# Optimization experiments

Hardware: AMD Instinct MI355X
Metric: run time of the kernel (lower is better)

Reference implementation:

```python
import jax, jax.numpy as jnp
import numpy as np

B, C, H, W = 1, 512, 64, 64
HEADS, DIM_HEAD = 8, 64
GROUPS = 32
EPS = 1e-5
SCALE = DIM_HEAD ** -0.5


def setup_inputs() -> dict:
    key = jax.random.key(0)
    ks = jax.random.split(key, 8)
    inner = HEADS * DIM_HEAD  # 512
    s = 0.02
    return {
        "hidden_states": jax.random.normal(ks[0], (B, C, H, W), jnp.float32),
        "gn_gamma": jnp.ones((C,), jnp.float32),
        "gn_beta": jnp.zeros((C,), jnp.float32),
        "wq": jax.random.normal(ks[1], (inner, C), jnp.float32) * s,
        "wk": jax.random.normal(ks[2], (inner, C), jnp.float32) * s,
        "wv": jax.random.normal(ks[3], (inner, C), jnp.float32) * s,
        "wo": jax.random.normal(ks[4], (C, inner), jnp.float32) * s,
        "bo": jnp.zeros((C,), jnp.float32),
    }


def _group_norm(x, gamma, beta):
    # x: [B, C, H, W]; normalize within channel groups over (C//G, H, W)
    b, c, h, w = x.shape
    xg = x.reshape(b, GROUPS, c // GROUPS, h, w)
    mean = xg.mean(axis=(2, 3, 4), keepdims=True)
    var = xg.var(axis=(2, 3, 4), keepdims=True)
    xg = (xg - mean) * jax.lax.rsqrt(var + EPS)
    x = xg.reshape(b, c, h, w)
    return x * gamma[None, :, None, None] + beta[None, :, None, None]


def reference(hidden_states, gn_gamma, gn_beta, wq, wk, wv, wo, bo):
    residual = hidden_states
    x = _group_norm(hidden_states, gn_gamma, gn_beta)
    b, c, h, w = x.shape
    n = h * w
    x = x.reshape(b, c, n).transpose(0, 2, 1)  # [B, N, C]

    # torch Linear: y = x @ W^T (bias=False for q/k/v)
    q = (x @ wq.T).reshape(b, n, HEADS, DIM_HEAD).transpose(0, 2, 1, 3)  # [B,H,N,D]
    k = (x @ wk.T).reshape(b, n, HEADS, DIM_HEAD).transpose(0, 2, 1, 3)
    v = (x @ wv.T).reshape(b, n, HEADS, DIM_HEAD).transpose(0, 2, 1, 3)

    scores = jnp.einsum("bhqd,bhkd->bhqk", q, k) * SCALE  # [B,H,N,N]
    probs = jax.nn.softmax(scores, axis=-1)
    out = jnp.einsum("bhqk,bhkd->bhqd", probs, v)  # [B,H,N,D]

    out = out.transpose(0, 2, 1, 3).reshape(b, n, HEADS * DIM_HEAD)  # [B,N,inner]
    out = out @ wo.T + bo  # [B,N,C]
    out = out.transpose(0, 2, 1).reshape(b, c, h, w)
    return out + residual
```

## Files before the change

kernel.cpp:

```cpp
#include <hip/hip_runtime.h>

#define N_TOK 4096
#define C_DIM 512
#define NH    8
#define EPS   1e-5f
#define NSPLIT 4
#define THR   11.0f

typedef __attribute__((ext_vector_type(8))) __bf16 bf16x8;
typedef __attribute__((ext_vector_type(4))) float  f32x4;
using u16 = unsigned short;
using u32 = unsigned int;

#define MFMA16 __builtin_amdgcn_mfma_f32_16x16x32_bf16

__device__ __forceinline__ u16 f2bf(float f){
  u32 x = __builtin_bit_cast(u32, f);
  x += 0x7fffu + ((x>>16)&1u);
  return (u16)(x>>16);
}
__device__ __forceinline__ float bf2f(u16 v){
  return __builtin_bit_cast(float, (u32)v<<16);
}
__device__ __forceinline__ float exp2a(float x){
  float r; asm("v_exp_f32 %0, %1" : "=v"(r) : "v"(x)); return r;
}
__device__ __forceinline__ u32 cvtpk(float lo, float hi){
  u32 r; asm("v_cvt_pk_bf16_f32 %0, %1, %2" : "=v"(r) : "v"(lo), "v"(hi)); return r;
}
__device__ __forceinline__ float max3a(float a, float b, float c){
  float r; asm("v_max3_f32 %0, %1, %2, %3" : "=v"(r) : "v"(a), "v"(b), "v"(c)); return r;
}
__device__ __forceinline__ void dma16(const void* src, void* lds){
  __builtin_amdgcn_global_load_lds(
      (const __attribute__((address_space(1))) u32*)src,
      (__attribute__((address_space(3))) u32*)lds, 16, 0, 0);
}

__global__ __launch_bounds__(256) void k_pre(const float* __restrict__ s0,
      const float* __restrict__ s1, const float* __restrict__ s2,
      const float* __restrict__ s3, u16* __restrict__ d0, u16* __restrict__ d1,
      u16* __restrict__ d2, u16* __restrict__ d3,
      const float* __restrict__ x, float* __restrict__ pstat,
      u16* __restrict__ xbf){
  __shared__ float rs[4], rss[4];
  int b = blockIdx.x;
  if (b < 1024){
    int m = b >> 8;
    int i = (b & 255)*256 + threadIdx.x;
    const float* s = m==0?s0 : m==1?s1 : m==2?s2 : s3;
    u16*         d = m==0?d0 : m==1?d1 : m==2?d2 : d3;
    float4 v = ((const float4*)s)[i];
    ushort4 o; o.x=f2bf(v.x); o.y=f2bf(v.y); o.z=f2bf(v.z); o.w=f2bf(v.w);
    ((ushort4*)d)[i] = o;
    return;
  }
  int gb = b - 1024;
  int g = gb>>3, p = gb&7, t = threadIdx.x;
  const float4* gx4 = (const float4*)(x + (size_t)g*16*N_TOK) + (size_t)p*2048;
  ushort4* xb4 = (ushort4*)xbf + (size_t)g*16384 + (size_t)p*2048;
  float s=0.f, ss=0.f;
  #pragma unroll
  for (int k=0;k<8;k++){
    float4 v = gx4[t + k*256];
    s  += v.x+v.y+v.z+v.w;
    ss += v.x*v.x+v.y*v.y+v.z*v.z+v.w*v.w;
    ushort4 o; o.x=f2bf(v.x); o.y=f2bf(v.y); o.z=f2bf(v.z); o.w=f2bf(v.w);
    xb4[t + k*256] = o;
  }
  for (int m=1;m<64;m<<=1){ s += __shfl_xor(s,m); ss += __shfl_xor(ss,m); }
  int w=t>>6, lane=t&63;
  if (lane==0){ rs[w]=s; rss[w]=ss; }
  __syncthreads();
  if (t==0){
    pstat[(g*8+p)*2  ] = rs[0]+rs[1]+rs[2]+rs[3];
    pstat[(g*8+p)*2+1] = rss[0]+rss[1]+rss[2]+rss[3];
  }
}

__global__ __launch_bounds__(256) void k_gn_apply(const u16* __restrict__ xbf,
      const float* __restrict__ pstat, const float* __restrict__ gamma,
      const float* __restrict__ beta, u16* __restrict__ X){
  int g = blockIdx.x, c0 = g*16;
  int n = blockIdx.y*256 + threadIdx.x;
  float S=0.f, SS=0.f;
  #pragma unroll
  for (int p=0;p<8;p++){ S += pstat[(g*8+p)*2]; SS += pstat[(g*8+p)*2+1]; }
  float mean = S*(1.f/65536.f);
  float rstd = rsqrtf(SS*(1.f/65536.f) - mean*mean + EPS);
  u16 ov[16];
  #pragma unroll
  for (int c=0;c<16;c++){
    float gm = gamma[c0+c]*rstd;
    float be = beta[c0+c] - mean*gm;
    float v  = bf2f(xbf[(size_t)(c0+c)*N_TOK + n])*gm + be;
    ov[c] = f2bf(v);
  }
  uint4* dst = (uint4*)&X[(size_t)n*C_DIM + c0];
  dst[0] = *(uint4*)&ov[0];
  dst[1] = *(uint4*)&ov[8];
}

__device__ __forceinline__ void gemm_core64(const u16* A, const u16* B,
      int m0, int n0, char* LDS, f32x4 (&acc)[4][2]){
  int t = threadIdx.x, w = t>>6, l = t&63, lr = l&15, li = l>>4;
  int wr = w>>1, wc = w&1;
  char* As = LDS;
  char* Bs = LDS + 32768;
  const char* Ac = (const char*)A + (size_t)m0*1024;
  const char* Bc = (const char*)B + (size_t)n0*1024;
  int rswz = (lr&7)<<4;

  int rowA[4], segA[4], rowB[2], segB[2];
  #pragma unroll
  for (int k=0;k<4;k++){ int s=t+k*256; rowA[k]=s>>3; segA[k]=s&7; }
  #pragma unroll
  for (int k=0;k<2;k++){ int s=t+k*256; rowB[k]=s>>3; segB[k]=s&7; }

  #define STAGE(it, bb) { int koff=(it)*128;                                   \
    _Pragma("unroll")                                                          \
    for (int k=0;k<4;k++){                                                     \
      int ys = (segA[k]*16) ^ ((rowA[k]&7)<<4);                                \
      dma16(Ac + (size_t)rowA[k]*1024 + koff + ys,                             \
            As + (bb)*16384 + w*1024 + k*4096);                                \
    }                                                                          \
    _Pragma("unroll")                                                          \
    for (int k=0;k<2;k++){                                                     \
      int ys = (segB[k]*16) ^ ((rowB[k]&7)<<4);                                \
      dma16(Bc + (size_t)rowB[k]*1024 + koff + ys,                             \
            Bs + (bb)*8192 + w*1024 + k*4096);                                 \
    } }

  STAGE(0, 0);
  __syncthreads();

  int buf = 0;
  for (int it=0; it<8; it++){
    if (it < 7){ STAGE(it+1, buf^1); }
    char* Ab = As + buf*16384;
    char* Bb = Bs + buf*8192;
    #pragma unroll
    for (int ks=0; ks<2; ks++){
      bf16x8 af[4], bfr[2];
      #pragma unroll
      for (int i=0;i<4;i++){
        int ra = wr*64 + i*16 + lr;
        af[i]  = *(const bf16x8*)(Ab + ra*128 + ((li*16 + ks*64) ^ rswz));
      }
      #pragma unroll
      for (int j=0;j<2;j++){
        int rb = wc*32 + j*16 + lr;
        bfr[j] = *(const bf16x8*)(Bb + rb*128 + ((li*16 + ks*64) ^ rswz));
      }
      __builtin_amdgcn_s_setprio(1);
      #pragma unroll
      for (int i=0;i<4;i++){
        #pragma unroll
        for (int j=0;j<2;j++){
          acc[i][j] = MFMA16(af[i], bfr[j], acc[i][j], 0,0,0);
        }
      }
      __builtin_amdgcn_s_setprio(0);
    }
    __syncthreads();
    buf ^= 1;
  }
  #undef STAGE
}

__global__ __launch_bounds__(256,3) void k_qkv2(const u16* __restrict__ X,
      const u16* __restrict__ wq, const u16* __restrict__ wk,
      const u16* __restrict__ wv, u16* __restrict__ Qo, u16* __restrict__ Ko,
      u16* __restrict__ Vto){
  __shared__ char LDS[49152];
  int b = blockIdx.x;
  const u16 *A, *B; u16* Cp; int ldc, m0, n0; float sc = 1.f; bool vperm = false;
  if (b < 256){        A=X;  B=wq; Cp=Qo;  ldc=512;  m0=(b>>3)*128; n0=(b&7)*64;
                       sc = 0.125f*1.44269504f; }
  else if (b < 512){ int r=b-256; A=X;  B=wk; Cp=Ko;  ldc=512;  m0=(r>>3)*128; n0=(r&7)*64; }
  else             { int r=b-512; A=wv; B=X;  Cp=Vto; ldc=4096; m0=(r>>6)*128; n0=(r&63)*64;
                     vperm = true; }

  f32x4 acc[4][2] = {};
  gemm_core64(A, B, m0, n0, LDS, acc);

  int t = threadIdx.x, w = t>>6, l = t&63, lr = l&15, li = l>>4;
  int wr = w>>1, wc = w&1;
  #pragma unroll
  for (int i=0;i<4;i++){
    #pragma unroll
    for (int rr=0;rr<4;rr++){
      int mm = m0 + wr*64 + i*16 + li*4 + rr;
      #pragma unroll
      for (int j=0;j<2;j++){
        int nn = n0 + wc*32 + j*16 + lr;
        if (vperm){
          int tl = nn & 63;
          int pos = (tl & 35) | ((tl & 12) << 1) | ((tl & 16) >> 2);
          nn = (nn & ~63) | pos;
        }
        Cp[(size_t)mm*ldc + nn] = f2bf(acc[i][j][rr]*sc);
      }
    }
  }
}

__global__ __launch_bounds__(256,3) void k_oproj2(const u16* __restrict__ Wo,
      const u16* __restrict__ Ob, const float* __restrict__ bo,
      const float* __restrict__ res, float* __restrict__ out){
  __shared__ char LDS[49152];
  int b = blockIdx.x;
  int m0 = (b>>6)*128, n0 = (b&63)*64;

  f32x4 acc[4][2] = {};
  gemm_core64(Wo, Ob, m0, n0, LDS, acc);

  int t = threadIdx.x, w = t>>6, l = t&63, lr = l&15, li = l>>4;
  int wr = w>>1, wc = w&1;
  #pragma unroll
  for (int i=0;i<4;i++){
    #pragma unroll
    for (int rr=0;rr<4;rr++){
      int cc = m0 + wr*64 + i*16 + li*4 + rr;
      float bias = bo[cc];
      #pragma unroll
      for (int j=0;j<2;j++){
        int nn = n0 + wc*32 + j*16 + lr;
        size_t off = (size_t)cc*4096 + nn;
        out[off] = acc[i][j][rr] + bias + res[off];
      }
    }
  }
}

__global__ __launch_bounds__(256,4) void k_attn6(const u16* __restrict__ Q,
      const u16* __restrict__ K, const u16* __restrict__ Vt,
      u16* __restrict__ Opart, float* __restrict__ ml){
  __shared__ char KV[2][16384];
  int b = blockIdx.x;
  int xcd  = b & 7;
  int slot = b >> 3;
  int pair = xcd*4 + (slot >> 5);
  int h  = pair & 7;
  int sp = pair >> 3;
  int q0 = (slot & 31) * 128;
  int t = threadIdx.x, w = t>>6, l = t&63, lr = l&15, li = l>>4;
  char* KVb = (char*)KV;
  int qbase = q0 + w*32;

  const u16* Qp = Q + (size_t)(qbase + lr)*512 + h*64 + li*8;
  bf16x8 qa00 = *(const bf16x8*)(Qp);
  bf16x8 qa01 = *(const bf16x8*)(Qp + 32);
  bf16x8 qa10 = *(const bf16x8*)(Qp + 16*512);
  bf16x8 qa11 = *(const bf16x8*)(Qp + 16*512 + 32);

  int srow = l>>3, y0 = (l&7)*16;
  const char* Kc = (const char*)K;
  const char* Vc = (const char*)Vt;
  const char* ksrc[2]; const char* vsrc[2]; int ldso[2];
  #pragma unroll
  for (int j=0;j<2;j++){
    int row = w*16 + j*8 + srow;
    int ys  = y0 ^ ((row&7)<<4);
    ksrc[j] = Kc + (size_t)(sp*1024 + row)*1024 + h*128 + ys;
    vsrc[j] = Vc + (size_t)(h*64 + row)*8192 + sp*2048 + ys;
    ldso[j] = w*2048 + j*1024;
  }

  #pragma unroll
  for (int j=0;j<2;j++){
    dma16(ksrc[j], KVb + ldso[j]);
    dma16(vsrc[j], KVb + 8192 + ldso[j]);
  }
  __syncthreads();

  f32x4 acc0[4] = {}; f32x4 acc1[4] = {};
  float m0=-1e30f, m1=-1e30f, l0=0.f, l1=0.f;
  int buf = 0;

  for (int it=0; it<16; it++){
    if (it < 15){
      int nb = buf^1;
      #pragma unroll
      for (int j=0;j<2;j++){
        dma16(ksrc[j] + (size_t)(it+1)*65536, KVb + nb*16384 + ldso[j]);
        dma16(vsrc[j] + (it+1)*128,           KVb + nb*16384 + 8192 + ldso[j]);
      }
    }
    char* Klb = KVb + buf*16384;
    char* Vlb = Klb + 8192;

    f32x4 st0[4] = {}; f32x4 st1[4] = {};
    __builtin_amdgcn_s_setprio(1);
    #pragma unroll
    for (int T=0;T<4;T++){
      int row = T*16 + lr, swz = (row&7)<<4;
      const char* rb = Klb + row*128;
      bf16x8 k0 = *(const bf16x8*)(rb + ((li*16     ) ^ swz));
      bf16x8 k1 = *(const bf16x8*)(rb + ((li*16 + 64) ^ swz));
      st0[T] = MFMA16(k0, qa00, st0[T], 0,0,0);
      st0[T] = MFMA16(k1, qa01, st0[T], 0,0,0);
      st1[T] = MFMA16(k0, qa10, st1[T], 0,0,0);
      st1[T] = MFMA16(k1, qa11, st1[T], 0,0,0);
    }
    __builtin_amdgcn_s_setprio(0);

    u32 pk0[8], pk1[8];
    {
      float a0 = max3a(st0[0][0],st0[0][1],st0[0][2]);
      float a1 = max3a(st0[1][0],st0[1][1],st0[1][2]);
      float a2 = max3a(st0[2][0],st0[2][1],st0[2][2]);
      float a3 = max3a(st0[3][0],st0[3][1],st0[3][2]);
      float b0 = max3a(st0[0][3],st0[1][3],st0[2][3]);
      float pmax = fmaxf(max3a(a0,a1,a2), max3a(a3,b0,st0[3][3]));
      pmax = fmaxf(pmax, __shfl_xor(pmax,16));
      pmax = fmaxf(pmax, __shfl_xor(pmax,32));
      if (!__all(pmax <= m0 + THR)){
        float mnew = fmaxf(m0, pmax);
        float fac = exp2a(m0 - mnew);
        m0 = mnew; l0 *= fac;
        float f0=__shfl(fac, li*20+0), f1=__shfl(fac, li*20+1);
        float f2=__shfl(fac, li*20+2), f3=__shfl(fac, li*20+3);
        #pragma unroll
        for (int T=0;T<4;T++){
          acc0[T][0]*=f0; acc0[T][1]*=f1; acc0[T][2]*=f2; acc0[T][3]*=f3;
        }
      }
      float lad = 0.f;
      #pragma unroll
      for (int T=0;T<4;T++){
        float p0=exp2a(st0[T][0]-m0), p1=exp2a(st0[T][1]-m0);
        float p2=exp2a(st0[T][2]-m0), p3=exp2a(st0[T][3]-m0);
        lad += (p0+p1)+(p2+p3);
        pk0[T*2]   = cvtpk(p0,p1);
        pk0[T*2+1] = cvtpk(p2,p3);
      }
      l0 += lad;
    }
    {
      float a0 = max3a(st1[0][0],st1[0][1],st1[0][2]);
      float a1 = max3a(st1[1][0],st1[1][1],st1[1][2]);
      float a2 = max3a(st1[2][0],st1[2][1],st1[2][2]);
      float a3 = max3a(st1[3][0],st1[3][1],st1[3][2]);
      float b0 = max3a(st1[0][3],st1[1][3],st1[2][3]);
      float pmax = fmaxf(max3a(a0,a1,a2), max3a(a3,b0,st1[3][3]));
      pmax = fmaxf(pmax, __shfl_xor(pmax,16));
      pmax = fmaxf(pmax, __shfl_xor(pmax,32));
      if (!__all(pmax <= m1 + THR)){
        float mnew = fmaxf(m1, pmax);
        float fac = exp2a(m1 - mnew);
        m1 = mnew; l1 *= fac;
        float f0=__shfl(fac, li*20+0), f1=__shfl(fac, li*20+1);
        float f2=__shfl(fac, li*20+2), f3=__shfl(fac, li*20+3);
        #pragma unroll
        for (int T=0;T<4;T++){
          acc1[T][0]*=f0; acc1[T][1]*=f1; acc1[T][2]*=f2; acc1[T][3]*=f3;
        }
      }
      float lad = 0.f;
      #pragma unroll
      for (int T=0;T<4;T++){
        float p0=exp2a(st1[T][0]-m1), p1=exp2a(st1[T][1]-m1);
        float p2=exp2a(st1[T][2]-m1), p3=exp2a(st1[T][3]-m1);
        lad += (p0+p1)+(p2+p3);
        pk1[T*2]   = cvtpk(p0,p1);
        pk1[T*2+1] = cvtpk(p2,p3);
      }
      l1 += lad;
    }

    __builtin_amdgcn_s_setprio(1);
    #pragma unroll
    for (int c=0;c<2;c++){
      union { bf16x8 v; u32 u[4]; } A0, A1;
      #pragma unroll
      for (int k=0;k<4;k++){ A0.u[k]=pk0[c*4+k]; A1.u[k]=pk1[c*4+k]; }
      #pragma unroll
      for (int T=0;T<4;T++){
        int vrow = T*16 + lr, vswz = (vrow&7)<<4;
        bf16x8 vb = *(const bf16x8*)(Vlb + vrow*128 + ((c*64 + li*16) ^ vswz));
        acc0[T] = MFMA16(A0.v, vb, acc0[T], 0,0,0);
        acc1[T] = MFMA16(A1.v, vb, acc1[T], 0,0,0);
      }
    }
    __builtin_amdgcn_s_setprio(0);

    __syncthreads();
    buf ^= 1;
  }

  l0 += __shfl_xor(l0,16); l0 += __shfl_xor(l0,32);
  l1 += __shfl_xor(l1,16); l1 += __shfl_xor(l1,32);
  u16* Op = Opart + (size_t)sp*N_TOK*C_DIM;
  #pragma unroll
  for (int T=0;T<4;T++){
    #pragma unroll
    for (int r=0;r<4;r++){
      Op[(size_t)(qbase      + li*4 + r)*512 + h*64 + T*16 + lr] = f2bf(acc0[T][r]);
      Op[(size_t)(qbase + 16 + li*4 + r)*512 + h*64 + T*16 + lr] = f2bf(acc1[T][r]);
    }
  }
  if (li==0){
    float* p0 = ml + (((size_t)sp*NH + h)*N_TOK + qbase + lr)*2;
    p0[0]=m0; p0[1]=l0;
    float* p1 = ml + (((size_t)sp*NH + h)*N_TOK + qbase + 16 + lr)*2;
    p1[0]=m1; p1[1]=l1;
  }
}

__global__ __launch_bounds__(256) void k_merge2(const u16* __restrict__ Opart,
      const float* __restrict__ ml, u16* __restrict__ Ob){
  int i  = blockIdx.x*256 + threadIdx.x;
  int q  = i >> 7;
  int c4 = i & 127;
  int h  = c4 >> 4;
  float m[NSPLIT], lv[NSPLIT];
  #pragma unroll
  for (int s=0;s<NSPLIT;s++){
    const float* p = ml + (((size_t)s*NH + h)*N_TOK + q)*2;
    m[s]=p[0]; lv[s]=p[1];
  }
  float M = fmaxf(max3a(m[0],m[1],m[2]), m[3]);
  float wgt[NSPLIT]; float L = 0.f;
  #pragma unroll
  for (int s=0;s<NSPLIT;s++){ wgt[s] = exp2a(m[s]-M); L += lv[s]*wgt[s]; }
  float inv = 1.f/L;
  float4 o = {0.f,0.f,0.f,0.f};
  #pragma unroll
  for (int s=0;s<NSPLIT;s++){
    ushort4 a = ((const ushort4*)(Opart + (size_t)s*N_TOK*C_DIM))[i];
    o.x += bf2f(a.x)*wgt[s]; o.y += bf2f(a.y)*wgt[s];
    o.z += bf2f(a.z)*wgt[s]; o.w += bf2f(a.w)*wgt[s];
  }
  ushort4 r;
  r.x=f2bf(o.x*inv); r.y=f2bf(o.y*inv); r.z=f2bf(o.z*inv); r.w=f2bf(o.w*inv);
  ((ushort4*)Ob)[i] = r;
}

extern "C" void kernel_launch(void* const* d_in, const int* in_sizes, int n_in,
                              void* d_out, int out_size, void* d_ws, size_t ws_size,
                              hipStream_t stream){
  (void)in_sizes; (void)n_in; (void)out_size; (void)ws_size;
  const float* hs    = (const float*)d_in[0];
  const float* gamma = (const float*)d_in[1];
  const float* beta  = (const float*)d_in[2];
  const float* wq    = (const float*)d_in[3];
  const float* wk    = (const float*)d_in[4];
  const float* wv    = (const float*)d_in[5];
  const float* wo    = (const float*)d_in[6];
  const float* bo    = (const float*)d_in[7];
  float* out = (float*)d_out;

  u16* X   = (u16*)d_ws;
  u16* Qb  = X   + (size_t)4096*512;
  u16* Kb  = Qb  + (size_t)4096*512;
  u16* Vtb = Kb  + (size_t)4096*512;
  u16* Ob  = Vtb + (size_t)4096*512;
  u16* xbf = Ob  + (size_t)4096*512;
  u16* wqb = xbf + (size_t)4096*512;
  u16* wkb = wqb + (size_t)512*512;
  u16* wvb = wkb + (size_t)512*512;
  u16* wob = wvb + (size_t)512*512;
  float* pstat = (float*)(wob + (size_t)512*512);
  u16* Opart   = (u16*)(pstat + 1024);
  float* mlbuf = (float*)(Opart + (size_t)NSPLIT*4096*512);

  k_pre<<<1280,256,0,stream>>>(wq, wk, wv, wo, wqb, wkb, wvb, wob, hs, pstat, xbf);
  dim3 ga(32, 16);
  k_gn_apply<<<ga,256,0,stream>>>(xbf, pstat, gamma, beta, X);
  k_qkv2<<<768,256,0,stream>>>(X, wqb, wkb, wvb, Qb, Kb, Vtb);
  k_attn6<<<1024,256,0,stream>>>(Qb, Kb, Vtb, Opart, mlbuf);
  k_merge2<<<2048,256,0,stream>>>(Opart, mlbuf, Ob);
  k_oproj2<<<256,256,0,stream>>>(wob, Ob, bo, hs, out);
}
```

Measured before the change: 86.11 us.

## Split attention work across 8 waves with 16 query rows each

The attention kernel now launches 512 threads per block, 8 waves each owning 16 query rows, instead of 4 waves each handling 32 rows as two 16-row tiles. Each thread issues one K and one V DMA per tile instead of two, and per-wave register state is halved (one accumulator set, one softmax state). The aim is more waves in flight per CU and lower register pressure. In exchange, each K/V load from LDS is reused by half as many MFMAs per wave, adding LDS read traffic and barrier participants.

```diff
diff --git a/kernel.cpp b/kernel.cpp
--- a/kernel.cpp
+++ b/kernel.cpp
@@ -233,7 +233,7 @@
   }
 }
 
-__global__ __launch_bounds__(256,4) void k_attn6(const u16* __restrict__ Q,
+__global__ __launch_bounds__(512,8) void k_attn8(const u16* __restrict__ Q,
       const u16* __restrict__ K, const u16* __restrict__ Vt,
       u16* __restrict__ Opart, float* __restrict__ ml){
   __shared__ char KV[2][16384];
@@ -246,73 +246,56 @@
   int q0 = (slot & 31) * 128;
   int t = threadIdx.x, w = t>>6, l = t&63, lr = l&15, li = l>>4;
   char* KVb = (char*)KV;
-  int qbase = q0 + w*32;
+  int qbase = q0 + w*16;
 
   const u16* Qp = Q + (size_t)(qbase + lr)*512 + h*64 + li*8;
-  bf16x8 qa00 = *(const bf16x8*)(Qp);
-  bf16x8 qa01 = *(const bf16x8*)(Qp + 32);
-  bf16x8 qa10 = *(const bf16x8*)(Qp + 16*512);
-  bf16x8 qa11 = *(const bf16x8*)(Qp + 16*512 + 32);
-
-  int srow = l>>3, y0 = (l&7)*16;
-  const char* Kc = (const char*)K;
-  const char* Vc = (const char*)Vt;
-  const char* ksrc[2]; const char* vsrc[2]; int ldso[2];
-  #pragma unroll
-  for (int j=0;j<2;j++){
-    int row = w*16 + j*8 + srow;
-    int ys  = y0 ^ ((row&7)<<4);
-    ksrc[j] = Kc + (size_t)(sp*1024 + row)*1024 + h*128 + ys;
-    vsrc[j] = Vc + (size_t)(h*64 + row)*8192 + sp*2048 + ys;
-    ldso[j] = w*2048 + j*1024;
-  }
-
-  #pragma unroll
-  for (int j=0;j<2;j++){
-    dma16(ksrc[j], KVb + ldso[j]);
-    dma16(vsrc[j], KVb + 8192 + ldso[j]);
-  }
+  bf16x8 qa0 = *(const bf16x8*)(Qp);
+  bf16x8 qa1 = *(const bf16x8*)(Qp + 32);
+
+  int row = t>>3, seg = t&7;
+  int ys  = (seg*16) ^ ((row&7)<<4);
+  const char* ksrc = (const char*)K  + (size_t)(sp*1024 + row)*1024 + h*128 + ys;
+  const char* vsrc = (const char*)Vt + (size_t)(h*64 + row)*8192 + sp*2048 + ys;
+  int ldso = w*1024;
+
+  dma16(ksrc, KVb + ldso);
+  dma16(vsrc, KVb + 8192 + ldso);
   __syncthreads();
 
-  f32x4 acc0[4] = {}; f32x4 acc1[4] = {};
-  float m0=-1e30f, m1=-1e30f, l0=0.f, l1=0.f;
+  f32x4 acc[4] = {};
+  float m0=-1e30f, l0=0.f;
   int buf = 0;
 
   for (int it=0; it<16; it++){
     if (it < 15){
       int nb = buf^1;
-      #pragma unroll
-      for (int j=0;j<2;j++){
-        dma16(ksrc[j] + (size_t)(it+1)*65536, KVb + nb*16384 + ldso[j]);
-        dma16(vsrc[j] + (it+1)*128,           KVb + nb*16384 + 8192 + ldso[j]);
-      }
+      dma16(ksrc + (size_t)(it+1)*65536, KVb + nb*16384 + ldso);
+      dma16(vsrc + (it+1)*128,           KVb + nb*16384 + 8192 + ldso);
     }
     char* Klb = KVb + buf*16384;
     char* Vlb = Klb + 8192;
 
-    f32x4 st0[4] = {}; f32x4 st1[4] = {};
+    f32x4 st[4] = {};
     __builtin_amdgcn_s_setprio(1);
     #pragma unroll
     for (int T=0;T<4;T++){
-      int row = T*16 + lr, swz = (row&7)<<4;
-      const char* rb = Klb + row*128;
+      int krow = T*16 + lr, swz = (krow&7)<<4;
+      const char* rb = Klb + krow*128;
       bf16x8 k0 = *(const bf16x8*)(rb + ((li*16     ) ^ swz));
       bf16x8 k1 = *(const bf16x8*)(rb + ((li*16 + 64) ^ swz));
-      st0[T] = MFMA16(k0, qa00, st0[T], 0,0,0);
-      st0[T] = MFMA16(k1, qa01, st0[T], 0,0,0);
-      st1[T] = MFMA16(k0, qa10, st1[T], 0,0,0);
-      st1[T] = MFMA16(k1, qa11, st1[T], 0,0,0);
+      st[T] = MFMA16(k0, qa0, st[T], 0,0,0);
+      st[T] = MFMA16(k1, qa1, st[T], 0,0,0);
     }
     __builtin_amdgcn_s_setprio(0);
 
-    u32 pk0[8], pk1[8];
+    u32 pk[8];
     {
-      float a0 = max3a(st0[0][0],st0[0][1],st0[0][2]);
-      float a1 = max3a(st0[1][0],st0[1][1],st0[1][2]);
-      float a2 = max3a(st0[2][0],st0[2][1],st0[2][2]);
-      float a3 = max3a(st0[3][0],st0[3][1],st0[3][2]);
-      float b0 = max3a(st0[0][3],st0[1][3],st0[2][3]);
-      float pmax = fmaxf(max3a(a0,a1,a2), max3a(a3,b0,st0[3][3]));
+      float a0 = max3a(st[0][0],st[0][1],st[0][2]);
+      float a1 = max3a(st[1][0],st[1][1],st[1][2]);
+      float a2 = max3a(st[2][0],st[2][1],st[2][2]);
+      float a3 = max3a(st[3][0],st[3][1],st[3][2]);
+      float b0 = max3a(st[0][3],st[1][3],st[2][3]);
+      float pmax = fmaxf(max3a(a0,a1,a2), max3a(a3,b0,st[3][3]));
       pmax = fmaxf(pmax, __shfl_xor(pmax,16));
       pmax = fmaxf(pmax, __shfl_xor(pmax,32));
       if (!__all(pmax <= m0 + THR)){
@@ -323,64 +306,32 @@
         float f2=__shfl(fac, li*20+2), f3=__shfl(fac, li*20+3);
         #pragma unroll
         for (int T=0;T<4;T++){
-          acc0[T][0]*=f0; acc0[T][1]*=f1; acc0[T][2]*=f2; acc0[T][3]*=f3;
+          acc[T][0]*=f0; acc[T][1]*=f1; acc[T][2]*=f2; acc[T][3]*=f3;
         }
       }
       float lad = 0.f;
       #pragma unroll
       for (int T=0;T<4;T++){
-        float p0=exp2a(st0[T][0]-m0), p1=exp2a(st0[T][1]-m0);
-        float p2=exp2a(st0[T][2]-m0), p3=exp2a(st0[T][3]-m0);
+        float p0=exp2a(st[T][0]-m0), p1=exp2a(st[T][1]-m0);
+        float p2=exp2a(st[T][2]-m0), p3=exp2a(st[T][3]-m0);
         lad += (p0+p1)+(p2+p3);
-        pk0[T*2]   = cvtpk(p0,p1);
-        pk0[T*2+1] = cvtpk(p2,p3);
+        pk[T*2]   = cvtpk(p0,p1);
+        pk[T*2+1] = cvtpk(p2,p3);
       }
       l0 += lad;
     }
-    {
-      float a0 = max3a(st1[0][0],st1[0][1],st1[0][2]);
-      float a1 = max3a(st1[1][0],st1[1][1],st1[1][2]);
-      float a2 = max3a(st1[2][0],st1[2][1],st1[2][2]);
-      float a3 = max3a(st1[3][0],st1[3][1],st1[3][2]);
-      float b0 = max3a(st1[0][3],st1[1][3],st1[2][3]);
-      float pmax = fmaxf(max3a(a0,a1,a2), max3a(a3,b0,st1[3][3]));
-      pmax = fmaxf(pmax, __shfl_xor(pmax,16));
-      pmax = fmaxf(pmax, __shfl_xor(pmax,32));
-      if (!__all(pmax <= m1 + THR)){
-        float mnew = fmaxf(m1, pmax);
-        float fac = exp2a(m1 - mnew);
-        m1 = mnew; l1 *= fac;
-        float f0=__shfl(fac, li*20+0), f1=__shfl(fac, li*20+1);
-        float f2=__shfl(fac, li*20+2), f3=__shfl(fac, li*20+3);
-        #pragma unroll
-        for (int T=0;T<4;T++){
-          acc1[T][0]*=f0; acc1[T][1]*=f1; acc1[T][2]*=f2; acc1[T][3]*=f3;
-        }
-      }
-      float lad = 0.f;
-      #pragma unroll
-      for (int T=0;T<4;T++){
-        float p0=exp2a(st1[T][0]-m1), p1=exp2a(st1[T][1]-m1);
-        float p2=exp2a(st1[T][2]-m1), p3=exp2a(st1[T][3]-m1);
-        lad += (p0+p1)+(p2+p3);
-        pk1[T*2]   = cvtpk(p0,p1);
-        pk1[T*2+1] = cvtpk(p2,p3);
-      }
-      l1 += lad;
-    }
 
     __builtin_amdgcn_s_setprio(1);
     #pragma unroll
     for (int c=0;c<2;c++){
-      union { bf16x8 v; u32 u[4]; } A0, A1;
-      #pragma unroll
-      for (int k=0;k<4;k++){ A0.u[k]=pk0[c*4+k]; A1.u[k]=pk1[c*4+k]; }
+      union { bf16x8 v; u32 u[4]; } A0;
+      #pragma unroll
+      for (int k=0;k<4;k++){ A0.u[k]=pk[c*4+k]; }
       #pragma unroll
       for (int T=0;T<4;T++){
         int vrow = T*16 + lr, vswz = (vrow&7)<<4;
         bf16x8 vb = *(const bf16x8*)(Vlb + vrow*128 + ((c*64 + li*16) ^ vswz));
-        acc0[T] = MFMA16(A0.v, vb, acc0[T], 0,0,0);
-        acc1[T] = MFMA16(A1.v, vb, acc1[T], 0,0,0);
+        acc[T] = MFMA16(A0.v, vb, acc[T], 0,0,0);
       }
     }
     __builtin_amdgcn_s_setprio(0);
@@ -390,21 +341,17 @@
   }
 
   l0 += __shfl_xor(l0,16); l0 += __shfl_xor(l0,32);
-  l1 += __shfl_xor(l1,16); l1 += __shfl_xor(l1,32);
   u16* Op = Opart + (size_t)sp*N_TOK*C_DIM;
   #pragma unroll
   for (int T=0;T<4;T++){
     #pragma unroll
     for (int r=0;r<4;r++){
-      Op[(size_t)(qbase      + li*4 + r)*512 + h*64 + T*16 + lr] = f2bf(acc0[T][r]);
-      Op[(size_t)(qbase + 16 + li*4 + r)*512 + h*64 + T*16 + lr] = f2bf(acc1[T][r]);
+      Op[(size_t)(qbase + li*4 + r)*512 + h*64 + T*16 + lr] = f2bf(acc[T][r]);
     }
   }
   if (li==0){
     float* p0 = ml + (((size_t)sp*NH + h)*N_TOK + qbase + lr)*2;
     p0[0]=m0; p0[1]=l0;
-    float* p1 = ml + (((size_t)sp*NH + h)*N_TOK + qbase + 16 + lr)*2;
-    p1[0]=m1; p1[1]=l1;
   }
 }
 
@@ -469,7 +416,7 @@
   dim3 ga(32, 16);
   k_gn_apply<<<ga,256,0,stream>>>(xbf, pstat, gamma, beta, X);
   k_qkv2<<<768,256,0,stream>>>(X, wqb, wkb, wvb, Qb, Kb, Vtb);
-  k_attn6<<<1024,256,0,stream>>>(Qb, Kb, Vtb, Opart, mlbuf);
+  k_attn8<<<1024,512,0,stream>>>(Qb, Kb, Vtb, Opart, mlbuf);
   k_merge2<<<2048,256,0,stream>>>(Opart, mlbuf, Ob);
   k_oproj2<<<256,256,0,stream>>>(wob, Ob, bo, hs, out);
 }
```

New measurement: 90.92 us. 1.06x slower.

## Deepen attention K/V prefetch to four LDS buffers with partial vmcnt waits

Applied to the files above, without the earlier changes.

The attention kernel now rotates through four LDS buffers and prefetches K/V tiles two iterations ahead instead of one. The full __syncthreads at the end of each iteration is replaced by a partial s_waitcnt vmcnt plus a raw barrier, so the next tile's DMA can stay in flight while compute continues. The aim is to hide global-memory latency better. The cost is 64KB of LDS per block, with launch bounds relaxed to 2 blocks per CU, which may lower occupancy.

```diff
diff --git a/kernel.cpp b/kernel.cpp
--- a/kernel.cpp
+++ b/kernel.cpp
@@ -233,10 +233,10 @@
   }
 }
 
-__global__ __launch_bounds__(256,4) void k_attn6(const u16* __restrict__ Q,
+__global__ __launch_bounds__(256,2) void k_attn10(const u16* __restrict__ Q,
       const u16* __restrict__ K, const u16* __restrict__ Vt,
       u16* __restrict__ Opart, float* __restrict__ ml){
-  __shared__ char KV[2][16384];
+  __shared__ char KV[4][16384];
   int b = blockIdx.x;
   int xcd  = b & 7;
   int slot = b >> 3;
@@ -272,22 +272,28 @@
     dma16(ksrc[j], KVb + ldso[j]);
     dma16(vsrc[j], KVb + 8192 + ldso[j]);
   }
-  __syncthreads();
+  #pragma unroll
+  for (int j=0;j<2;j++){
+    dma16(ksrc[j] + 65536, KVb + 16384 + ldso[j]);
+    dma16(vsrc[j] + 128,   KVb + 16384 + 8192 + ldso[j]);
+  }
+  asm volatile("s_waitcnt vmcnt(4)" ::: "memory");
+  __builtin_amdgcn_s_barrier();
+  __builtin_amdgcn_sched_barrier(0);
 
   f32x4 acc0[4] = {}; f32x4 acc1[4] = {};
   float m0=-1e30f, m1=-1e30f, l0=0.f, l1=0.f;
-  int buf = 0;
 
   for (int it=0; it<16; it++){
-    if (it < 15){
-      int nb = buf^1;
+    if (it < 14){
+      char* nbuf = KVb + ((it+2)&3)*16384;
       #pragma unroll
       for (int j=0;j<2;j++){
-        dma16(ksrc[j] + (size_t)(it+1)*65536, KVb + nb*16384 + ldso[j]);
-        dma16(vsrc[j] + (it+1)*128,           KVb + nb*16384 + 8192 + ldso[j]);
-      }
-    }
-    char* Klb = KVb + buf*16384;
+        dma16(ksrc[j] + (size_t)(it+2)*65536, nbuf + ldso[j]);
+        dma16(vsrc[j] + (it+2)*128,           nbuf + 8192 + ldso[j]);
+      }
+    }
+    char* Klb = KVb + (it&3)*16384;
     char* Vlb = Klb + 8192;
 
     f32x4 st0[4] = {}; f32x4 st1[4] = {};
@@ -385,8 +391,12 @@
     }
     __builtin_amdgcn_s_setprio(0);
 
-    __syncthreads();
-    buf ^= 1;
+    if (it < 15){
+      if (it < 14){ asm volatile("s_waitcnt vmcnt(4)" ::: "memory"); }
+      else        { asm volatile("s_waitcnt vmcnt(0)" ::: "memory"); }
+      __builtin_amdgcn_s_barrier();
+      __builtin_amdgcn_sched_barrier(0);
+    }
   }
 
   l0 += __shfl_xor(l0,16); l0 += __shfl_xor(l0,32);
@@ -469,7 +479,7 @@
   dim3 ga(32, 16);
   k_gn_apply<<<ga,256,0,stream>>>(xbf, pstat, gamma, beta, X);
   k_qkv2<<<768,256,0,stream>>>(X, wqb, wkb, wvb, Qb, Kb, Vtb);
-  k_attn6<<<1024,256,0,stream>>>(Qb, Kb, Vtb, Opart, mlbuf);
+  k_attn10<<<1024,256,0,stream>>>(Qb, Kb, Vtb, Opart, mlbuf);
   k_merge2<<<2048,256,0,stream>>>(Opart, mlbuf, Ob);
   k_oproj2<<<256,256,0,stream>>>(wob, Ob, bo, hs, out);
 }
```

Measured after the change: 89.91 us. +4.4%, slower.
